# Performance work log

Hardware: AMD Instinct MI355X
Metric: run time of the kernel (lower is better)

## Reference

```python
import jax, jax.numpy as jnp
import numpy as np

N_NODES, N_EDGES = 16384, 8192
IN_CH, HID_CH = 256, 256
ALPHA, BETA = -1.5, -0.5


def setup_inputs() -> dict:
    key = jax.random.key(0)
    k1, k2, k3, k4, k5, k6 = jax.random.split(key, 6)
    x_0 = jax.random.normal(k1, (N_NODES, IN_CH), dtype=jnp.float32)
    # binary incidence matrix (n_nodes, n_edges)
    incidence_1 = jax.random.randint(k2, (N_NODES, N_EDGES), 0, 2).astype(jnp.float32)
    # conv weights (torch Conv: x @ W then neighborhood @ .)
    W0 = jax.random.normal(k3, (IN_CH, HID_CH), dtype=jnp.float32) * 0.02
    W1 = jax.random.normal(k4, (HID_CH, HID_CH), dtype=jnp.float32) * 0.02
    # xavier_uniform biases of shape (1, hidden)
    gain = 1.414
    bound = gain * np.sqrt(6.0 / (1 + HID_CH)) * np.sqrt(3.0) / np.sqrt(3.0)  # xavier bound = gain*sqrt(6/(fan_in+fan_out))
    bound = gain * np.sqrt(6.0 / (1 + HID_CH))
    bias_0_to_1 = jax.random.uniform(k5, (1, HID_CH), minval=-bound, maxval=bound, dtype=jnp.float32)
    bias_1_to_0 = jax.random.uniform(k6, (1, HID_CH), minval=-bound, maxval=bound, dtype=jnp.float32)
    return {"x_0": x_0, "incidence_1": incidence_1, "W0": W0, "W1": W1,
            "bias_0_to_1": bias_0_to_1, "bias_1_to_0": bias_1_to_0}


def _normalize_incidence(B1):
    # edge/node cardinalities raised to alpha/beta
    edge_card = jnp.sum(B1, axis=0) ** ALPHA          # (n_edges,)
    node_card = jnp.sum(B1, axis=1) ** BETA           # (n_nodes,)
    mask = (B1 > 0).astype(B1.dtype)
    d0_inv = 1.0 / (mask @ edge_card)                 # (n_nodes,) per-node sum of incident edge_card
    d1_inv = 1.0 / (mask.T @ node_card)               # (n_edges,) per-edge sum of member node_card
    # B1_norm = D0_left^-1 @ B1 @ diag(edge_card)
    B1_norm = d0_inv[:, None] * B1 * edge_card[None, :]
    # B1T_norm = D1_left^-1 @ B1^T @ diag(node_card)
    B1T_norm = d1_inv[:, None] * B1.T * node_card[None, :]
    return B1_norm, B1T_norm


def reference(x_0, incidence_1, W0, W1, bias_0_to_1, bias_1_to_0):
    B1_norm, B1T_norm = _normalize_incidence(incidence_1)
    # node -> edge conv: x_1 = B1T_norm @ (x_0 @ W0) + b01
    x_1 = B1T_norm @ (x_0 @ W0) + bias_0_to_1        # (n_edges, hid)
    # edge -> node conv: x_0 = B1_norm @ (x_1 @ W1) + b10
    x_0_out = B1_norm @ (x_1 @ W1) + bias_1_to_0     # (n_nodes, hid)
    return jax.nn.relu(x_0_out), jax.nn.relu(x_1)
```

## Files before the change

kernel.cpp:

```cpp
#include <hip/hip_runtime.h>
#include <stdint.h>

#define NN 16384
#define NE 8192
#define CH 256
#define MM1_SPLIT 8
#define MM2_SPLIT 4

typedef __attribute__((ext_vector_type(8))) short bf16x8;
typedef __attribute__((ext_vector_type(4))) float f32x4;

__device__ __forceinline__ unsigned short f2bf(float f) {
  unsigned u = __float_as_uint(f);
  u += 0x7FFFu + ((u >> 16) & 1u);
  return (unsigned short)(u >> 16);
}
__device__ __forceinline__ void async_copy16(const void* gptr, void* lptr) {
  __builtin_amdgcn_global_load_lds((const __attribute__((address_space(1))) unsigned int*)gptr,
                                   (__attribute__((address_space(3))) unsigned int*)lptr,
                                   16, 0, 0);
}
__device__ __forceinline__ uint4 expand8(unsigned byte) {
  uint4 aw;
#pragma unroll
  for (int j = 0; j < 4; ++j) {
    unsigned lo = (byte >> (2 * j)) & 1u;
    unsigned hi = (byte >> (2 * j + 1)) & 1u;
    ((unsigned*)&aw)[j] = lo * 0x3F80u + hi * 0x3F800000u;
  }
  return aw;
}

__device__ __forceinline__ void transpose32(unsigned* x) {
  const unsigned masks[5] = {0x0000FFFFu, 0x00FF00FFu, 0x0F0F0F0Fu, 0x33333333u, 0x55555555u};
#pragma unroll
  for (int jj = 0; jj < 5; ++jj) {
    const int j = 16 >> jj;
    const unsigned m = masks[jj];
#pragma unroll
    for (int k = 0; k < 32; ++k) {
      if ((k & j) == 0) {
        unsigned t = ((x[k] >> j) ^ x[k + j]) & m;
        x[k] ^= (t << j);
        x[k + j] ^= t;
      }
    }
  }
}

__global__ void k0_transpose_w(const float* __restrict__ W0, const float* __restrict__ W1,
                               unsigned short* __restrict__ W0T, unsigned short* __restrict__ W1T) {
  const float* W = blockIdx.y ? W1 : W0;
  unsigned short* WT = blockIdx.y ? W1T : W0T;
  int n = blockIdx.x;
  int k = threadIdx.x;
  WT[n * CH + k] = f2bf(W[k * CH + n]);
}

__global__ void k1_pack_card(const float* __restrict__ B1, unsigned* __restrict__ pk1,
                             float* __restrict__ node_card) {
  int n = blockIdx.x;
  int t = threadIdx.x;
  const float4* p = (const float4*)(B1 + (size_t)n * NE + t * 32);
  unsigned w = 0;
#pragma unroll
  for (int jj = 0; jj < 8; ++jj) {
    float4 v = p[jj];
    w |= ((__float_as_uint(v.x) >> 23) & 1u) << (4 * jj);
    w |= ((__float_as_uint(v.y) >> 23) & 1u) << (4 * jj + 1);
    w |= ((__float_as_uint(v.z) >> 23) & 1u) << (4 * jj + 2);
    w |= ((__float_as_uint(v.w) >> 23) & 1u) << (4 * jj + 3);
  }
  pk1[(size_t)n * 256 + t] = w;
  int s = __popc(w);
  __shared__ int red[4];
#pragma unroll
  for (int off = 32; off; off >>= 1) s += __shfl_down(s, off, 64);
  if ((t & 63) == 0) red[t >> 6] = s;
  __syncthreads();
  if (t == 0) {
    float tot = (float)(red[0] + red[1] + red[2] + red[3]);
    node_card[n] = rsqrtf(tot);
  }
}

__global__ __launch_bounds__(256) void k1b_bitT(const unsigned* __restrict__ pk1,
                                                unsigned* __restrict__ pk1T) {
  int bw = blockIdx.x & 127;
  int half = blockIdx.x >> 7;
  int t = threadIdx.x;
  int nt = half * 256 + t;
  unsigned x0[32], x1[32];
#pragma unroll
  for (int r = 0; r < 32; ++r) {
    uint2 v = *(const uint2*)&pk1[(size_t)(nt * 32 + r) * 256 + 2 * bw];
    x0[r] = v.x;
    x1[r] = v.y;
  }
  transpose32(x0);
  transpose32(x1);
  int e0 = bw * 64;
#pragma unroll
  for (int c = 0; c < 32; ++c) {
    pk1T[(size_t)(e0 + c) * 512 + nt] = x0[c];
    pk1T[(size_t)(e0 + 32 + c) * 512 + nt] = x1[c];
  }
}

__global__ __launch_bounds__(256) void ke_edge(const unsigned* __restrict__ pk1T,
                                               const float* __restrict__ node_card,
                                               float* __restrict__ edge_card,
                                               float* __restrict__ d1) {
  const int t = threadIdx.x;
  const int e0 = blockIdx.x * 4;
  unsigned w[4][2];
#pragma unroll
  for (int r = 0; r < 4; ++r) {
    w[r][0] = pk1T[(size_t)(e0 + r) * 512 + t];
    w[r][1] = pk1T[(size_t)(e0 + r) * 512 + 256 + t];
  }
  float wsum[4] = {0.f, 0.f, 0.f, 0.f};
  int cnt[4];
#pragma unroll
  for (int r = 0; r < 4; ++r) cnt[r] = __popc(w[r][0]) + __popc(w[r][1]);
  const float4* nc0 = (const float4*)(node_card + (size_t)t * 32);
  const float4* nc1 = (const float4*)(node_card + ((size_t)t + 256) * 32);
#pragma unroll
  for (int h = 0; h < 2; ++h) {
    const float4* ncp = h ? nc1 : nc0;
#pragma unroll
    for (int q = 0; q < 8; ++q) {
      float4 v = ncp[q];
#pragma unroll
      for (int r = 0; r < 4; ++r) {
        unsigned ww = w[r][h];
        wsum[r] += ((ww >> (4 * q)) & 1u) ? v.x : 0.f;
        wsum[r] += ((ww >> (4 * q + 1)) & 1u) ? v.y : 0.f;
        wsum[r] += ((ww >> (4 * q + 2)) & 1u) ? v.z : 0.f;
        wsum[r] += ((ww >> (4 * q + 3)) & 1u) ? v.w : 0.f;
      }
    }
  }
#pragma unroll
  for (int off = 32; off; off >>= 1)
#pragma unroll
    for (int r = 0; r < 4; ++r) {
      wsum[r] += __shfl_down(wsum[r], off, 64);
      cnt[r] += __shfl_down(cnt[r], off, 64);
    }
  __shared__ float redW[4][4];
  __shared__ int redC[4][4];
  int wave = t >> 6, lane = t & 63;
  if (lane == 0)
#pragma unroll
    for (int r = 0; r < 4; ++r) {
      redW[wave][r] = wsum[r];
      redC[wave][r] = cnt[r];
    }
  __syncthreads();
  if (t < 4) {
    float s = redW[0][t] + redW[1][t] + redW[2][t] + redW[3][t];
    float c = (float)(redC[0][t] + redC[1][t] + redC[2][t] + redC[3][t]);
    d1[e0 + t] = s;
    edge_card[e0 + t] = 1.0f / (c * sqrtf(c));
  }
}

__global__ __launch_bounds__(256) void kd0_node(const unsigned* __restrict__ pk1,
                                                const float* __restrict__ edge_card,
                                                float* __restrict__ d0) {
  const int t = threadIdx.x;
  const int n0 = blockIdx.x * 4;
  unsigned w[4];
#pragma unroll
  for (int r = 0; r < 4; ++r) w[r] = pk1[(size_t)(n0 + r) * 256 + t];
  float wsum[4] = {0.f, 0.f, 0.f, 0.f};
  const float4* ecp = (const float4*)(edge_card + (size_t)t * 32);
#pragma unroll
  for (int q = 0; q < 8; ++q) {
    float4 v = ecp[q];
#pragma unroll
    for (int r = 0; r < 4; ++r) {
      unsigned ww = w[r];
      wsum[r] += ((ww >> (4 * q)) & 1u) ? v.x : 0.f;
      wsum[r] += ((ww >> (4 * q + 1)) & 1u) ? v.y : 0.f;
      wsum[r] += ((ww >> (4 * q + 2)) & 1u) ? v.z : 0.f;
      wsum[r] += ((ww >> (4 * q + 3)) & 1u) ? v.w : 0.f;
    }
  }
#pragma unroll
  for (int off = 32; off; off >>= 1)
#pragma unroll
    for (int r = 0; r < 4; ++r) wsum[r] += __shfl_down(wsum[r], off, 64);
  __shared__ float redW[4][4];
  int wave = t >> 6, lane = t & 63;
  if (lane == 0)
#pragma unroll
    for (int r = 0; r < 4; ++r) redW[wave][r] = wsum[r];
  __syncthreads();
  if (t < 4) d0[n0 + t] = redW[0][t] + redW[1][t] + redW[2][t] + redW[3][t];
}

__global__ __launch_bounds__(256) void k2_y0(const float* __restrict__ X0,
                                             const unsigned short* __restrict__ W0T,
                                             const float* __restrict__ node_card,
                                             unsigned short* __restrict__ y0sT) {
  __shared__ __align__(16) unsigned short a_lds[32 * 32];
  __shared__ __align__(16) unsigned short b_lds[256 * 32];
  const int tid = threadIdx.x;
  const int wave = tid >> 6, lane = tid & 63;
  const int quad = lane >> 4, l15 = lane & 15;
  const int m0 = blockIdx.x * 32;
  const int ar = tid >> 3, ac = (tid & 7) * 4;

  f32x4 acc[2][4];
  const f32x4 fz = {0.f, 0.f, 0.f, 0.f};
#pragma unroll
  for (int i = 0; i < 2; ++i)
#pragma unroll
    for (int j = 0; j < 4; ++j) acc[i][j] = fz;

  for (int k0 = 0; k0 < CH; k0 += 32) {
    __syncthreads();
    {
      float4 v = *(const float4*)(X0 + (size_t)(m0 + ar) * CH + k0 + ac);
      uint2 w;
      w.x = ((unsigned)f2bf(v.x)) | ((unsigned)f2bf(v.y) << 16);
      w.y = ((unsigned)f2bf(v.z)) | ((unsigned)f2bf(v.w) << 16);
      *(uint2*)&a_lds[ar * 32 + ac] = w;
    }
#pragma unroll
    for (int i = 0; i < 4; ++i) {
      int rowbase = wave * 64 + i * 16;
      const unsigned short* g = W0T + (size_t)(rowbase + (lane >> 2)) * CH + k0 + (lane & 3) * 8;
      async_copy16(g, &b_lds[rowbase * 32]);
    }
    __syncthreads();
    bf16x8 af[2];
#pragma unroll
    for (int i = 0; i < 2; ++i)
      af[i] = *(const bf16x8*)&a_lds[(i * 16 + l15) * 32 + quad * 8];
#pragma unroll
    for (int j = 0; j < 4; ++j) {
      bf16x8 bfr = *(const bf16x8*)&b_lds[(wave * 64 + j * 16 + l15) * 32 + quad * 8];
#pragma unroll
      for (int i = 0; i < 2; ++i)
        acc[i][j] = __builtin_amdgcn_mfma_f32_16x16x32_bf16(af[i], bfr, acc[i][j], 0, 0, 0);
    }
  }
#pragma unroll
  for (int i = 0; i < 2; ++i) {
    int row4 = m0 + i * 16 + quad * 4;
    float4 nc = *(const float4*)(node_card + row4);
#pragma unroll
    for (int j = 0; j < 4; ++j) {
      int col = wave * 64 + j * 16 + l15;
      f32x4 v = acc[i][j];
      ushort4 o;
      o.x = f2bf(v[0] * nc.x);
      o.y = f2bf(v[1] * nc.y);
      o.z = f2bf(v[2] * nc.z);
      o.w = f2bf(v[3] * nc.w);
      *(ushort4*)&y0sT[(size_t)col * NN + row4] = o;
    }
  }
}

__global__ __launch_bounds__(512, 4) void mm1_kernel(const unsigned char* __restrict__ pk1T,
                                                     const unsigned short* __restrict__ y0sT,
                                                     float* __restrict__ mm1p) {
  __shared__ __align__(16) unsigned short b_lds[2][256 * 32];
  const int tid = threadIdx.x;
  const int wave = tid >> 6, lane = tid & 63;
  const int quad = lane >> 4, l15 = lane & 15;
  const int wm = wave >> 2, wn = wave & 3;
  const int bid = blockIdx.x;
  const int sp = bid & 7;
  const int m0 = (bid >> 3) * 128;
  const int KS = NN / MM1_SPLIT;
  const int NT = KS / 32;
  const int kbase = sp * KS;
  const int AST = NN / 8;

  const int brow = lane >> 2;
  const int bcol = (lane & 3) * 8;

  f32x4 acc[4][4];
  const f32x4 fz = {0.f, 0.f, 0.f, 0.f};
#pragma unroll
  for (int i = 0; i < 4; ++i)
#pragma unroll
    for (int j = 0; j < 4; ++j) acc[i][j] = fz;

  const unsigned char* abase = pk1T + (size_t)(m0 + wm * 64 + l15) * AST + (kbase >> 3) + quad;
  unsigned ab[4];
#pragma unroll
  for (int i = 0; i < 4; ++i) ab[i] = abase[(size_t)(i * 16) * AST];

#pragma unroll
  for (int i = 0; i < 2; ++i) {
    int rowbase = wave * 32 + i * 16;
    const unsigned short* g = y0sT + (size_t)(rowbase + brow) * NN + kbase + bcol;
    async_copy16(g, &b_lds[0][rowbase * 32]);
  }
  __syncthreads();

  for (int t = 0; t < NT; ++t) {
    const int cur = t & 1;
    if (t + 1 < NT) {
      const int k0n = kbase + (t + 1) * 32;
#pragma unroll
      for (int i = 0; i < 2; ++i) {
        int rowbase = wave * 32 + i * 16;
        const unsigned short* g = y0sT + (size_t)(rowbase + brow) * NN + k0n + bcol;
        async_copy16(g, &b_lds[cur ^ 1][rowbase * 32]);
      }
    }
    bf16x8 af[4];
#pragma unroll
    for (int i = 0; i < 4; ++i) {
      uint4 ue = expand8(ab[i]);
      af[i] = *reinterpret_cast<bf16x8*>(&ue);
    }
    if (t + 1 < NT) {
#pragma unroll
      for (int i = 0; i < 4; ++i) ab[i] = abase[(size_t)(i * 16) * AST + (t + 1) * 4];
    }
    __builtin_amdgcn_s_setprio(1);
#pragma unroll
    for (int j = 0; j < 4; ++j) {
      bf16x8 bfr = *(const bf16x8*)&b_lds[cur][(wn * 64 + j * 16 + l15) * 32 + quad * 8];
#pragma unroll
      for (int i = 0; i < 4; ++i)
        acc[i][j] = __builtin_amdgcn_mfma_f32_16x16x32_bf16(af[i], bfr, acc[i][j], 0, 0, 0);
    }
    __builtin_amdgcn_s_setprio(0);
    __syncthreads();
  }
  float* outp = mm1p + (size_t)sp * NE * CH;
#pragma unroll
  for (int i = 0; i < 4; ++i) {
    int row4 = m0 + wm * 64 + i * 16 + quad * 4;
#pragma unroll
    for (int j = 0; j < 4; ++j) {
      int col = wn * 64 + j * 16 + l15;
#pragma unroll
      for (int r = 0; r < 4; ++r) outp[(size_t)(row4 + r) * CH + col] = acc[i][j][r];
    }
  }
}

__global__ __launch_bounds__(256) void k3_edge_final(const float* __restrict__ mm1p,
                                                     const float* __restrict__ d1,
                                                     const float* __restrict__ b01,
                                                     float* __restrict__ out1,
                                                     unsigned short* __restrict__ x1bf) {
  const int t = threadIdx.x;
  const int e = blockIdx.x * 4 + (t >> 6);
  const int c4 = (t & 63) * 4;
  float px = 0.f, py = 0.f, pz = 0.f, pw = 0.f;
#pragma unroll
  for (int sp = 0; sp < MM1_SPLIT; ++sp) {
    float4 v = *(const float4*)&mm1p[(size_t)sp * NE * CH + (size_t)e * CH + c4];
    px += v.x; py += v.y; pz += v.z; pw += v.w;
  }
  const float rd = 1.0f / d1[e];
  const float4 b = *(const float4*)&b01[c4];
  float4 x1;
  x1.x = px * rd + b.x;
  x1.y = py * rd + b.y;
  x1.z = pz * rd + b.z;
  x1.w = pw * rd + b.w;
  float4 o;
  o.x = fmaxf(x1.x, 0.f); o.y = fmaxf(x1.y, 0.f);
  o.z = fmaxf(x1.z, 0.f); o.w = fmaxf(x1.w, 0.f);
  *(float4*)&out1[(size_t)e * CH + c4] = o;
  ushort4 xb;
  xb.x = f2bf(x1.x); xb.y = f2bf(x1.y); xb.z = f2bf(x1.z); xb.w = f2bf(x1.w);
  *(ushort4*)&x1bf[(size_t)e * CH + c4] = xb;
}

__global__ __launch_bounds__(256) void k5_y1(const unsigned short* __restrict__ x1bf,
                                             const unsigned short* __restrict__ W1T,
                                             const float* __restrict__ edge_card,
                                             unsigned short* __restrict__ y1sT) {
  __shared__ __align__(16) unsigned short a_lds[32 * 32];
  __shared__ __align__(16) unsigned short b_lds[256 * 32];
  const int tid = threadIdx.x;
  const int wave = tid >> 6, lane = tid & 63;
  const int quad = lane >> 4, l15 = lane & 15;
  const int m0 = blockIdx.x * 32;

  f32x4 acc[2][4];
  const f32x4 fz = {0.f, 0.f, 0.f, 0.f};
#pragma unroll
  for (int i = 0; i < 2; ++i)
#pragma unroll
    for (int j = 0; j < 4; ++j) acc[i][j] = fz;

  for (int k0 = 0; k0 < CH; k0 += 32) {
    __syncthreads();
    if (wave < 2) {
      const unsigned short* g = x1bf + (size_t)(m0 + wave * 16 + (lane >> 2)) * CH + k0 + (lane & 3) * 8;
      async_copy16(g, &a_lds[(wave * 16) * 32]);
    }
#pragma unroll
    for (int i = 0; i < 4; ++i) {
      int rowbase = wave * 64 + i * 16;
      const unsigned short* g = W1T + (size_t)(rowbase + (lane >> 2)) * CH + k0 + (lane & 3) * 8;
      async_copy16(g, &b_lds[rowbase * 32]);
    }
    __syncthreads();
    bf16x8 af[2];
#pragma unroll
    for (int i = 0; i < 2; ++i)
      af[i] = *(const bf16x8*)&a_lds[(i * 16 + l15) * 32 + quad * 8];
#pragma unroll
    for (int j = 0; j < 4; ++j) {
      bf16x8 bfr = *(const bf16x8*)&b_lds[(wave * 64 + j * 16 + l15) * 32 + quad * 8];
#pragma unroll
      for (int i = 0; i < 2; ++i)
        acc[i][j] = __builtin_amdgcn_mfma_f32_16x16x32_bf16(af[i], bfr, acc[i][j], 0, 0, 0);
    }
  }
#pragma unroll
  for (int i = 0; i < 2; ++i) {
    int row4 = m0 + i * 16 + quad * 4;
    float4 ec = *(const float4*)(edge_card + row4);
#pragma unroll
    for (int j = 0; j < 4; ++j) {
      int col = wave * 64 + j * 16 + l15;
      f32x4 v = acc[i][j];
      ushort4 o;
      o.x = f2bf(v[0] * ec.x);
      o.y = f2bf(v[1] * ec.y);
      o.z = f2bf(v[2] * ec.z);
      o.w = f2bf(v[3] * ec.w);
      *(ushort4*)&y1sT[(size_t)col * NE + row4] = o;
    }
  }
}

__global__ __launch_bounds__(512, 4) void mm2_kernel(const unsigned char* __restrict__ pk1,
                                                     const unsigned short* __restrict__ y1sT,
                                                     float* __restrict__ mm2p) {
  __shared__ __align__(16) unsigned short b_lds[2][256 * 32];
  const int tid = threadIdx.x;
  const int wave = tid >> 6, lane = tid & 63;
  const int quad = lane >> 4, l15 = lane & 15;
  const int wm = wave >> 2, wn = wave & 3;
  const int bid = blockIdx.x;
  const int sp = (bid >> 1) & 3;
  const int m0 = (((bid >> 3) << 1) | (bid & 1)) * 128;
  const int KS = NE / MM2_SPLIT;
  const int NT = KS / 32;
  const int kbase = sp * KS;
  const int AST = NE / 8;

  const int brow = lane >> 2;
  const int bcol = (lane & 3) * 8;

  f32x4 acc[4][4];
  const f32x4 fz = {0.f, 0.f, 0.f, 0.f};
#pragma unroll
  for (int i = 0; i < 4; ++i)
#pragma unroll
    for (int j = 0; j < 4; ++j) acc[i][j] = fz;

  const unsigned char* abase = pk1 + (size_t)(m0 + wm * 64 + l15) * AST + (kbase >> 3) + quad;
  unsigned ab[4];
#pragma unroll
  for (int i = 0; i < 4; ++i) ab[i] = abase[(size_t)(i * 16) * AST];

#pragma unroll
  for (int i = 0; i < 2; ++i) {
    int rowbase = wave * 32 + i * 16;
    const unsigned short* g = y1sT + (size_t)(rowbase + brow) * NE + kbase + bcol;
    async_copy16(g, &b_lds[0][rowbase * 32]);
  }
  __syncthreads();

  for (int t = 0; t < NT; ++t) {
    const int cur = t & 1;
    if (t + 1 < NT) {
      const int k0n = kbase + (t + 1) * 32;
#pragma unroll
      for (int i = 0; i < 2; ++i) {
        int rowbase = wave * 32 + i * 16;
        const unsigned short* g = y1sT + (size_t)(rowbase + brow) * NE + k0n + bcol;
        async_copy16(g, &b_lds[cur ^ 1][rowbase * 32]);
      }
    }
    bf16x8 af[4];
#pragma unroll
    for (int i = 0; i < 4; ++i) {
      uint4 ue = expand8(ab[i]);
      af[i] = *reinterpret_cast<bf16x8*>(&ue);
    }
    if (t + 1 < NT) {
#pragma unroll
      for (int i = 0; i < 4; ++i) ab[i] = abase[(size_t)(i * 16) * AST + (t + 1) * 4];
    }
    __builtin_amdgcn_s_setprio(1);
#pragma unroll
    for (int j = 0; j < 4; ++j) {
      bf16x8 bfr = *(const bf16x8*)&b_lds[cur][(wn * 64 + j * 16 + l15) * 32 + quad * 8];
#pragma unroll
      for (int i = 0; i < 4; ++i)
        acc[i][j] = __builtin_amdgcn_mfma_f32_16x16x32_bf16(af[i], bfr, acc[i][j], 0, 0, 0);
    }
    __builtin_amdgcn_s_setprio(0);
    __syncthreads();
  }
  float* outp = mm2p + (size_t)sp * NN * CH;
#pragma unroll
  for (int i = 0; i < 4; ++i) {
    int row4 = m0 + wm * 64 + i * 16 + quad * 4;
#pragma unroll
    for (int j = 0; j < 4; ++j) {
      int col = wn * 64 + j * 16 + l15;
#pragma unroll
      for (int r = 0; r < 4; ++r) outp[(size_t)(row4 + r) * CH + col] = acc[i][j][r];
    }
  }
}

__global__ __launch_bounds__(256) void k6_node_final(const float* __restrict__ mm2p,
                                                     const float* __restrict__ d0,
                                                     const float* __restrict__ b10,
                                                     float* __restrict__ out0) {
  const int t = threadIdx.x;
  const int n = blockIdx.x * 4 + (t >> 6);
  const int c4 = (t & 63) * 4;
  float sx = 0.f, sy = 0.f, sz = 0.f, sw = 0.f;
#pragma unroll
  for (int sp = 0; sp < MM2_SPLIT; ++sp) {
    float4 v = *(const float4*)&mm2p[(size_t)sp * NN * CH + (size_t)n * CH + c4];
    sx += v.x; sy += v.y; sz += v.z; sw += v.w;
  }
  const float rd = 1.0f / d0[n];
  const float4 b = *(const float4*)&b10[c4];
  float4 o;
  o.x = fmaxf(sx * rd + b.x, 0.f);
  o.y = fmaxf(sy * rd + b.y, 0.f);
  o.z = fmaxf(sz * rd + b.z, 0.f);
  o.w = fmaxf(sw * rd + b.w, 0.f);
  *(float4*)&out0[(size_t)n * CH + c4] = o;
}

extern "C" void kernel_launch(void* const* d_in, const int* in_sizes, int n_in,
                              void* d_out, int out_size, void* d_ws, size_t ws_size,
                              hipStream_t stream) {
  const float* x0 = (const float*)d_in[0];
  const float* B1 = (const float*)d_in[1];
  const float* W0 = (const float*)d_in[2];
  const float* W1 = (const float*)d_in[3];
  const float* b01 = (const float*)d_in[4];
  const float* b10 = (const float*)d_in[5];
  float* out0 = (float*)d_out;
  float* out1 = out0 + (size_t)NN * CH;

  char* ws = (char*)d_ws;
  size_t off = 0;
  auto take = [&](size_t bytes) {
    void* p = ws + off;
    off += (bytes + 255) & ~(size_t)255;
    return p;
  };
  unsigned short* y0sT = (unsigned short*)take((size_t)256 * NN * 2);
  unsigned short* y1sT = (unsigned short*)take((size_t)256 * NE * 2);
  unsigned short* x1bf = (unsigned short*)take((size_t)NE * CH * 2);
  float* mm1p = (float*)take((size_t)MM1_SPLIT * NE * CH * 4);
  float* mm2p = mm1p;
  float* node_card = (float*)take((size_t)NN * 4);
  float* edge_card = (float*)take((size_t)NE * 4);
  float* d1 = (float*)take((size_t)NE * 4);
  float* d0 = (float*)take((size_t)NN * 4);
  unsigned short* W0T = (unsigned short*)take((size_t)CH * CH * 2);
  unsigned short* W1T = (unsigned short*)take((size_t)CH * CH * 2);
  unsigned* pk1 = (unsigned*)take((size_t)NN * 256 * 4);
  unsigned* pk1T = (unsigned*)take((size_t)NE * 512 * 4);
  (void)ws_size; (void)in_sizes; (void)n_in; (void)out_size;

  k0_transpose_w<<<dim3(256, 2), 256, 0, stream>>>(W0, W1, W0T, W1T);
  k1_pack_card<<<NN, 256, 0, stream>>>(B1, pk1, node_card);
  k1b_bitT<<<256, 256, 0, stream>>>(pk1, pk1T);
  ke_edge<<<NE / 4, 256, 0, stream>>>(pk1T, node_card, edge_card, d1);
  kd0_node<<<NN / 4, 256, 0, stream>>>(pk1, edge_card, d0);
  k2_y0<<<NN / 32, 256, 0, stream>>>(x0, W0T, node_card, y0sT);
  mm1_kernel<<<512, 512, 0, stream>>>((const unsigned char*)pk1T, y0sT, mm1p);
  k3_edge_final<<<NE / 4, 256, 0, stream>>>(mm1p, d1, b01, out1, x1bf);
  k5_y1<<<NE / 32, 256, 0, stream>>>(x1bf, W1T, edge_card, y1sT);
  mm2_kernel<<<512, 512, 0, stream>>>((const unsigned char*)pk1, y1sT, mm2p);
  k6_node_final<<<NN / 4, 256, 0, stream>>>(mm2p, d0, b10, out0);
}
```

Measured before the change: 1.122 ms.

## Switch bit-packed GEMMs to 32x32x16 MFMA with shared-expanded A tile in LDS

```diff
diff --git a/kernel.cpp b/kernel.cpp
--- a/kernel.cpp
+++ b/kernel.cpp
@@ -9,6 +9,7 @@
 
 typedef __attribute__((ext_vector_type(8))) short bf16x8;
 typedef __attribute__((ext_vector_type(4))) float f32x4;
+typedef __attribute__((ext_vector_type(16))) float f32x16;
 
 __device__ __forceinline__ unsigned short f2bf(float f) {
   unsigned u = __float_as_uint(f);
@@ -269,10 +270,11 @@
 __global__ __launch_bounds__(512, 4) void mm1_kernel(const unsigned char* __restrict__ pk1T,
                                                      const unsigned short* __restrict__ y0sT,
                                                      float* __restrict__ mm1p) {
+  __shared__ __align__(16) unsigned short a_lds[2][128 * 40];
   __shared__ __align__(16) unsigned short b_lds[2][256 * 32];
   const int tid = threadIdx.x;
   const int wave = tid >> 6, lane = tid & 63;
-  const int quad = lane >> 4, l15 = lane & 15;
+  const int l31 = lane & 31, half = lane >> 5;
   const int wm = wave >> 2, wn = wave & 3;
   const int bid = blockIdx.x;
   const int sp = bid & 7;
@@ -280,22 +282,31 @@
   const int KS = NN / MM1_SPLIT;
   const int NT = KS / 32;
   const int kbase = sp * KS;
-  const int AST = NN / 8;
-
+
+  const int am = tid >> 2;
+  const int akg = tid & 3;
+  const int ajbs = akg ^ ((am >> 4) & 3);
+  const int aoff = am * 40 + ajbs * 8;
   const int brow = lane >> 2;
   const int bcol = (lane & 3) * 8;
 
-  f32x4 acc[4][4];
-  const f32x4 fz = {0.f, 0.f, 0.f, 0.f};
-#pragma unroll
-  for (int i = 0; i < 4; ++i)
-#pragma unroll
-    for (int j = 0; j < 4; ++j) acc[i][j] = fz;
-
-  const unsigned char* abase = pk1T + (size_t)(m0 + wm * 64 + l15) * AST + (kbase >> 3) + quad;
-  unsigned ab[4];
-#pragma unroll
-  for (int i = 0; i < 4; ++i) ab[i] = abase[(size_t)(i * 16) * AST];
+  const int arow0 = wm * 64 + l31;
+  const int arow1 = wm * 64 + 32 + l31;
+  const int as0 = (arow0 >> 4) & 3;
+  const int as1 = (arow1 >> 4) & 3;
+
+  f32x16 acc[2][2];
+#pragma unroll
+  for (int r = 0; r < 2; ++r)
+#pragma unroll
+    for (int c = 0; c < 2; ++c)
+#pragma unroll
+      for (int q = 0; q < 16; ++q) acc[r][c][q] = 0.f;
+
+  const unsigned char* agp = pk1T + (size_t)(m0 + am) * (NN / 8) + (kbase >> 3) + akg;
+  unsigned ab_cur = agp[0];
+  unsigned ab_nxt = agp[4];
+  const unsigned char* agq = agp + 8;
 
 #pragma unroll
   for (int i = 0; i < 2; ++i) {
@@ -303,10 +314,12 @@
     const unsigned short* g = y0sT + (size_t)(rowbase + brow) * NN + kbase + bcol;
     async_copy16(g, &b_lds[0][rowbase * 32]);
   }
+  *(uint4*)&a_lds[0][aoff] = expand8(ab_cur);
   __syncthreads();
 
   for (int t = 0; t < NT; ++t) {
     const int cur = t & 1;
+    unsigned ab_new = 0;
     if (t + 1 < NT) {
       const int k0n = kbase + (t + 1) * 32;
 #pragma unroll
@@ -315,39 +328,40 @@
         const unsigned short* g = y0sT + (size_t)(rowbase + brow) * NN + k0n + bcol;
         async_copy16(g, &b_lds[cur ^ 1][rowbase * 32]);
       }
-    }
-    bf16x8 af[4];
-#pragma unroll
-    for (int i = 0; i < 4; ++i) {
-      uint4 ue = expand8(ab[i]);
-      af[i] = *reinterpret_cast<bf16x8*>(&ue);
-    }
-    if (t + 1 < NT) {
-#pragma unroll
-      for (int i = 0; i < 4; ++i) ab[i] = abase[(size_t)(i * 16) * AST + (t + 1) * 4];
-    }
-    __builtin_amdgcn_s_setprio(1);
-#pragma unroll
-    for (int j = 0; j < 4; ++j) {
-      bf16x8 bfr = *(const bf16x8*)&b_lds[cur][(wn * 64 + j * 16 + l15) * 32 + quad * 8];
-#pragma unroll
-      for (int i = 0; i < 4; ++i)
-        acc[i][j] = __builtin_amdgcn_mfma_f32_16x16x32_bf16(af[i], bfr, acc[i][j], 0, 0, 0);
-    }
-    __builtin_amdgcn_s_setprio(0);
+      *(uint4*)&a_lds[cur ^ 1][aoff] = expand8(ab_nxt);
+      if (t + 2 < NT) {
+        ab_new = *agq;
+        agq += 4;
+      }
+    }
+#pragma unroll
+    for (int kb = 0; kb < 2; ++kb) {
+      const int kg = kb * 2 + half;
+      bf16x8 af0 = *(const bf16x8*)&a_lds[cur][arow0 * 40 + (kg ^ as0) * 8];
+      bf16x8 af1 = *(const bf16x8*)&a_lds[cur][arow1 * 40 + (kg ^ as1) * 8];
+      bf16x8 bf0 = *(const bf16x8*)&b_lds[cur][(wn * 64 + l31) * 32 + kg * 8];
+      bf16x8 bf1 = *(const bf16x8*)&b_lds[cur][(wn * 64 + 32 + l31) * 32 + kg * 8];
+      acc[0][0] = __builtin_amdgcn_mfma_f32_32x32x16_bf16(af0, bf0, acc[0][0], 0, 0, 0);
+      acc[1][0] = __builtin_amdgcn_mfma_f32_32x32x16_bf16(af1, bf0, acc[1][0], 0, 0, 0);
+      acc[0][1] = __builtin_amdgcn_mfma_f32_32x32x16_bf16(af0, bf1, acc[0][1], 0, 0, 0);
+      acc[1][1] = __builtin_amdgcn_mfma_f32_32x32x16_bf16(af1, bf1, acc[1][1], 0, 0, 0);
+    }
     __syncthreads();
+    ab_cur = ab_nxt;
+    ab_nxt = ab_new;
   }
   float* outp = mm1p + (size_t)sp * NE * CH;
 #pragma unroll
-  for (int i = 0; i < 4; ++i) {
-    int row4 = m0 + wm * 64 + i * 16 + quad * 4;
-#pragma unroll
-    for (int j = 0; j < 4; ++j) {
-      int col = wn * 64 + j * 16 + l15;
-#pragma unroll
-      for (int r = 0; r < 4; ++r) outp[(size_t)(row4 + r) * CH + col] = acc[i][j][r];
-    }
-  }
+  for (int r = 0; r < 2; ++r)
+#pragma unroll
+    for (int c = 0; c < 2; ++c) {
+      const int col = wn * 64 + c * 32 + l31;
+#pragma unroll
+      for (int reg = 0; reg < 16; ++reg) {
+        const int row = m0 + wm * 64 + r * 32 + (reg & 3) + 8 * (reg >> 2) + 4 * half;
+        outp[(size_t)row * CH + col] = acc[r][c][reg];
+      }
+    }
 }
 
 __global__ __launch_bounds__(256) void k3_edge_final(const float* __restrict__ mm1p,
@@ -444,10 +458,11 @@
 __global__ __launch_bounds__(512, 4) void mm2_kernel(const unsigned char* __restrict__ pk1,
                                                      const unsigned short* __restrict__ y1sT,
                                                      float* __restrict__ mm2p) {
+  __shared__ __align__(16) unsigned short a_lds[2][128 * 40];
   __shared__ __align__(16) unsigned short b_lds[2][256 * 32];
   const int tid = threadIdx.x;
   const int wave = tid >> 6, lane = tid & 63;
-  const int quad = lane >> 4, l15 = lane & 15;
+  const int l31 = lane & 31, half = lane >> 5;
   const int wm = wave >> 2, wn = wave & 3;
   const int bid = blockIdx.x;
   const int sp = (bid >> 1) & 3;
@@ -455,22 +470,31 @@
   const int KS = NE / MM2_SPLIT;
   const int NT = KS / 32;
   const int kbase = sp * KS;
-  const int AST = NE / 8;
-
+
+  const int am = tid >> 2;
+  const int akg = tid & 3;
+  const int ajbs = akg ^ ((am >> 4) & 3);
+  const int aoff = am * 40 + ajbs * 8;
   const int brow = lane >> 2;
   const int bcol = (lane & 3) * 8;
 
-  f32x4 acc[4][4];
-  const f32x4 fz = {0.f, 0.f, 0.f, 0.f};
-#pragma unroll
-  for (int i = 0; i < 4; ++i)
-#pragma unroll
-    for (int j = 0; j < 4; ++j) acc[i][j] = fz;
-
-  const unsigned char* abase = pk1 + (size_t)(m0 + wm * 64 + l15) * AST + (kbase >> 3) + quad;
-  unsigned ab[4];
-#pragma unroll
-  for (int i = 0; i < 4; ++i) ab[i] = abase[(size_t)(i * 16) * AST];
+  const int arow0 = wm * 64 + l31;
+  const int arow1 = wm * 64 + 32 + l31;
+  const int as0 = (arow0 >> 4) & 3;
+  const int as1 = (arow1 >> 4) & 3;
+
+  f32x16 acc[2][2];
+#pragma unroll
+  for (int r = 0; r < 2; ++r)
+#pragma unroll
+    for (int c = 0; c < 2; ++c)
+#pragma unroll
+      for (int q = 0; q < 16; ++q) acc[r][c][q] = 0.f;
+
+  const unsigned char* agp = pk1 + (size_t)(m0 + am) * (NE / 8) + (kbase >> 3) + akg;
+  unsigned ab_cur = agp[0];
+  unsigned ab_nxt = agp[4];
+  const unsigned char* agq = agp + 8;
 
 #pragma unroll
   for (int i = 0; i < 2; ++i) {
@@ -478,10 +502,12 @@
     const unsigned short* g = y1sT + (size_t)(rowbase + brow) * NE + kbase + bcol;
     async_copy16(g, &b_lds[0][rowbase * 32]);
   }
+  *(uint4*)&a_lds[0][aoff] = expand8(ab_cur);
   __syncthreads();
 
   for (int t = 0; t < NT; ++t) {
     const int cur = t & 1;
+    unsigned ab_new = 0;
     if (t + 1 < NT) {
       const int k0n = kbase + (t + 1) * 32;
 #pragma unroll
@@ -490,39 +516,40 @@
         const unsigned short* g = y1sT + (size_t)(rowbase + brow) * NE + k0n + bcol;
         async_copy16(g, &b_lds[cur ^ 1][rowbase * 32]);
       }
-    }
-    bf16x8 af[4];
-#pragma unroll
-    for (int i = 0; i < 4; ++i) {
-      uint4 ue = expand8(ab[i]);
-      af[i] = *reinterpret_cast<bf16x8*>(&ue);
-    }
-    if (t + 1 < NT) {
-#pragma unroll
-      for (int i = 0; i < 4; ++i) ab[i] = abase[(size_t)(i * 16) * AST + (t + 1) * 4];
-    }
-    __builtin_amdgcn_s_setprio(1);
-#pragma unroll
-    for (int j = 0; j < 4; ++j) {
-      bf16x8 bfr = *(const bf16x8*)&b_lds[cur][(wn * 64 + j * 16 + l15) * 32 + quad * 8];
-#pragma unroll
-      for (int i = 0; i < 4; ++i)
-        acc[i][j] = __builtin_amdgcn_mfma_f32_16x16x32_bf16(af[i], bfr, acc[i][j], 0, 0, 0);
-    }
-    __builtin_amdgcn_s_setprio(0);
+      *(uint4*)&a_lds[cur ^ 1][aoff] = expand8(ab_nxt);
+      if (t + 2 < NT) {
+        ab_new = *agq;
+        agq += 4;
+      }
+    }
+#pragma unroll
+    for (int kb = 0; kb < 2; ++kb) {
+      const int kg = kb * 2 + half;
+      bf16x8 af0 = *(const bf16x8*)&a_lds[cur][arow0 * 40 + (kg ^ as0) * 8];
+      bf16x8 af1 = *(const bf16x8*)&a_lds[cur][arow1 * 40 + (kg ^ as1) * 8];
+      bf16x8 bf0 = *(const bf16x8*)&b_lds[cur][(wn * 64 + l31) * 32 + kg * 8];
+      bf16x8 bf1 = *(const bf16x8*)&b_lds[cur][(wn * 64 + 32 + l31) * 32 + kg * 8];
+      acc[0][0] = __builtin_amdgcn_mfma_f32_32x32x16_bf16(af0, bf0, acc[0][0], 0, 0, 0);
+      acc[1][0] = __builtin_amdgcn_mfma_f32_32x32x16_bf16(af1, bf0, acc[1][0], 0, 0, 0);
+      acc[0][1] = __builtin_amdgcn_mfma_f32_32x32x16_bf16(af0, bf1, acc[0][1], 0, 0, 0);
+      acc[1][1] = __builtin_amdgcn_mfma_f32_32x32x16_bf16(af1, bf1, acc[1][1], 0, 0, 0);
+    }
     __syncthreads();
+    ab_cur = ab_nxt;
+    ab_nxt = ab_new;
   }
   float* outp = mm2p + (size_t)sp * NN * CH;
 #pragma unroll
-  for (int i = 0; i < 4; ++i) {
-    int row4 = m0 + wm * 64 + i * 16 + quad * 4;
-#pragma unroll
-    for (int j = 0; j < 4; ++j) {
-      int col = wn * 64 + j * 16 + l15;
-#pragma unroll
-      for (int r = 0; r < 4; ++r) outp[(size_t)(row4 + r) * CH + col] = acc[i][j][r];
-    }
-  }
+  for (int r = 0; r < 2; ++r)
+#pragma unroll
+    for (int c = 0; c < 2; ++c) {
+      const int col = wn * 64 + c * 32 + l31;
+#pragma unroll
+      for (int reg = 0; reg < 16; ++reg) {
+        const int row = m0 + wm * 64 + r * 32 + (reg & 3) + 8 * (reg >> 2) + 4 * half;
+        outp[(size_t)row * CH + col] = acc[r][c][reg];
+      }
+    }
 }
 
 __global__ __launch_bounds__(256) void k6_node_final(const float* __restrict__ mm2p,
```

New measurement: 983.2 us. -12.3%, faster.

## Swizzle LDS tiles and stage expanded incidence bits through shared memory

Applied to the files above, without the earlier changes.

```diff
diff --git a/kernel.cpp b/kernel.cpp
--- a/kernel.cpp
+++ b/kernel.cpp
@@ -212,6 +212,9 @@
   const int quad = lane >> 4, l15 = lane & 15;
   const int m0 = blockIdx.x * 32;
   const int ar = tid >> 3, ac = (tid & 7) * 4;
+  const int acs = (((ac >> 3) ^ ((ar >> 1) & 3)) * 8) + (ac & 4);
+  const int bswz = ((lane & 3) ^ ((lane >> 3) & 3)) * 8;
+  const int rg = (l15 >> 1) & 3;
 
   f32x4 acc[2][4];
   const f32x4 fz = {0.f, 0.f, 0.f, 0.f};
@@ -227,22 +230,22 @@
       uint2 w;
       w.x = ((unsigned)f2bf(v.x)) | ((unsigned)f2bf(v.y) << 16);
       w.y = ((unsigned)f2bf(v.z)) | ((unsigned)f2bf(v.w) << 16);
-      *(uint2*)&a_lds[ar * 32 + ac] = w;
+      *(uint2*)&a_lds[ar * 32 + acs] = w;
     }
 #pragma unroll
     for (int i = 0; i < 4; ++i) {
       int rowbase = wave * 64 + i * 16;
-      const unsigned short* g = W0T + (size_t)(rowbase + (lane >> 2)) * CH + k0 + (lane & 3) * 8;
+      const unsigned short* g = W0T + (size_t)(rowbase + (lane >> 2)) * CH + k0 + bswz;
       async_copy16(g, &b_lds[rowbase * 32]);
     }
     __syncthreads();
     bf16x8 af[2];
 #pragma unroll
     for (int i = 0; i < 2; ++i)
-      af[i] = *(const bf16x8*)&a_lds[(i * 16 + l15) * 32 + quad * 8];
-#pragma unroll
-    for (int j = 0; j < 4; ++j) {
-      bf16x8 bfr = *(const bf16x8*)&b_lds[(wave * 64 + j * 16 + l15) * 32 + quad * 8];
+      af[i] = *(const bf16x8*)&a_lds[(i * 16 + l15) * 32 + (quad ^ rg) * 8];
+#pragma unroll
+    for (int j = 0; j < 4; ++j) {
+      bf16x8 bfr = *(const bf16x8*)&b_lds[(wave * 64 + j * 16 + l15) * 32 + (quad ^ rg) * 8];
 #pragma unroll
       for (int i = 0; i < 2; ++i)
         acc[i][j] = __builtin_amdgcn_mfma_f32_16x16x32_bf16(af[i], bfr, acc[i][j], 0, 0, 0);
@@ -269,6 +272,7 @@
 __global__ __launch_bounds__(512, 4) void mm1_kernel(const unsigned char* __restrict__ pk1T,
                                                      const unsigned short* __restrict__ y0sT,
                                                      float* __restrict__ mm1p) {
+  __shared__ __align__(16) unsigned short a_lds[2][128 * 40];
   __shared__ __align__(16) unsigned short b_lds[2][256 * 32];
   const int tid = threadIdx.x;
   const int wave = tid >> 6, lane = tid & 63;
@@ -280,10 +284,14 @@
   const int KS = NN / MM1_SPLIT;
   const int NT = KS / 32;
   const int kbase = sp * KS;
-  const int AST = NN / 8;
-
+
+  const int am = tid >> 2;
+  const int akg = tid & 3;
+  const int ajbs = akg ^ ((am >> 4) & 3);
+  const int aoff = am * 40 + ajbs * 8;
   const int brow = lane >> 2;
-  const int bcol = (lane & 3) * 8;
+  const int bswz = ((lane & 3) ^ ((lane >> 3) & 3)) * 8;
+  const int rg = (l15 >> 1) & 3;
 
   f32x4 acc[4][4];
   const f32x4 fz = {0.f, 0.f, 0.f, 0.f};
@@ -292,50 +300,54 @@
 #pragma unroll
     for (int j = 0; j < 4; ++j) acc[i][j] = fz;
 
-  const unsigned char* abase = pk1T + (size_t)(m0 + wm * 64 + l15) * AST + (kbase >> 3) + quad;
-  unsigned ab[4];
-#pragma unroll
-  for (int i = 0; i < 4; ++i) ab[i] = abase[(size_t)(i * 16) * AST];
+  const unsigned char* agp = pk1T + (size_t)(m0 + am) * (NN / 8) + (kbase >> 3) + akg;
+  unsigned ab_cur = agp[0];
+  unsigned ab_nxt = agp[4];
+  const unsigned char* agq = agp + 8;
 
 #pragma unroll
   for (int i = 0; i < 2; ++i) {
     int rowbase = wave * 32 + i * 16;
-    const unsigned short* g = y0sT + (size_t)(rowbase + brow) * NN + kbase + bcol;
+    const unsigned short* g = y0sT + (size_t)(rowbase + brow) * NN + kbase + bswz;
     async_copy16(g, &b_lds[0][rowbase * 32]);
   }
+  *(uint4*)&a_lds[0][aoff] = expand8(ab_cur);
   __syncthreads();
 
   for (int t = 0; t < NT; ++t) {
     const int cur = t & 1;
+    unsigned ab_new = 0;
     if (t + 1 < NT) {
       const int k0n = kbase + (t + 1) * 32;
 #pragma unroll
       for (int i = 0; i < 2; ++i) {
         int rowbase = wave * 32 + i * 16;
-        const unsigned short* g = y0sT + (size_t)(rowbase + brow) * NN + k0n + bcol;
+        const unsigned short* g = y0sT + (size_t)(rowbase + brow) * NN + k0n + bswz;
         async_copy16(g, &b_lds[cur ^ 1][rowbase * 32]);
       }
+      *(uint4*)&a_lds[cur ^ 1][aoff] = expand8(ab_nxt);
+      if (t + 2 < NT) {
+        ab_new = *agq;
+        agq += 4;
+      }
     }
     bf16x8 af[4];
 #pragma unroll
     for (int i = 0; i < 4; ++i) {
-      uint4 ue = expand8(ab[i]);
-      af[i] = *reinterpret_cast<bf16x8*>(&ue);
-    }
-    if (t + 1 < NT) {
-#pragma unroll
-      for (int i = 0; i < 4; ++i) ab[i] = abase[(size_t)(i * 16) * AST + (t + 1) * 4];
-    }
-    __builtin_amdgcn_s_setprio(1);
-#pragma unroll
-    for (int j = 0; j < 4; ++j) {
-      bf16x8 bfr = *(const bf16x8*)&b_lds[cur][(wn * 64 + j * 16 + l15) * 32 + quad * 8];
+      int m = wm * 64 + i * 16 + l15;
+      int jbs = quad ^ ((m >> 4) & 3);
+      af[i] = *(const bf16x8*)&a_lds[cur][m * 40 + jbs * 8];
+    }
+#pragma unroll
+    for (int j = 0; j < 4; ++j) {
+      bf16x8 bfr = *(const bf16x8*)&b_lds[cur][(wn * 64 + j * 16 + l15) * 32 + (quad ^ rg) * 8];
 #pragma unroll
       for (int i = 0; i < 4; ++i)
         acc[i][j] = __builtin_amdgcn_mfma_f32_16x16x32_bf16(af[i], bfr, acc[i][j], 0, 0, 0);
     }
-    __builtin_amdgcn_s_setprio(0);
     __syncthreads();
+    ab_cur = ab_nxt;
+    ab_nxt = ab_new;
   }
   float* outp = mm1p + (size_t)sp * NE * CH;
 #pragma unroll
@@ -390,6 +402,8 @@
   const int wave = tid >> 6, lane = tid & 63;
   const int quad = lane >> 4, l15 = lane & 15;
   const int m0 = blockIdx.x * 32;
+  const int bswz = ((lane & 3) ^ ((lane >> 3) & 3)) * 8;
+  const int rg = (l15 >> 1) & 3;
 
   f32x4 acc[2][4];
   const f32x4 fz = {0.f, 0.f, 0.f, 0.f};
@@ -401,23 +415,23 @@
   for (int k0 = 0; k0 < CH; k0 += 32) {
     __syncthreads();
     if (wave < 2) {
-      const unsigned short* g = x1bf + (size_t)(m0 + wave * 16 + (lane >> 2)) * CH + k0 + (lane & 3) * 8;
+      const unsigned short* g = x1bf + (size_t)(m0 + wave * 16 + (lane >> 2)) * CH + k0 + bswz;
       async_copy16(g, &a_lds[(wave * 16) * 32]);
     }
 #pragma unroll
     for (int i = 0; i < 4; ++i) {
       int rowbase = wave * 64 + i * 16;
-      const unsigned short* g = W1T + (size_t)(rowbase + (lane >> 2)) * CH + k0 + (lane & 3) * 8;
+      const unsigned short* g = W1T + (size_t)(rowbase + (lane >> 2)) * CH + k0 + bswz;
       async_copy16(g, &b_lds[rowbase * 32]);
     }
     __syncthreads();
     bf16x8 af[2];
 #pragma unroll
     for (int i = 0; i < 2; ++i)
-      af[i] = *(const bf16x8*)&a_lds[(i * 16 + l15) * 32 + quad * 8];
-#pragma unroll
-    for (int j = 0; j < 4; ++j) {
-      bf16x8 bfr = *(const bf16x8*)&b_lds[(wave * 64 + j * 16 + l15) * 32 + quad * 8];
+      af[i] = *(const bf16x8*)&a_lds[(i * 16 + l15) * 32 + (quad ^ rg) * 8];
+#pragma unroll
+    for (int j = 0; j < 4; ++j) {
+      bf16x8 bfr = *(const bf16x8*)&b_lds[(wave * 64 + j * 16 + l15) * 32 + (quad ^ rg) * 8];
 #pragma unroll
       for (int i = 0; i < 2; ++i)
         acc[i][j] = __builtin_amdgcn_mfma_f32_16x16x32_bf16(af[i], bfr, acc[i][j], 0, 0, 0);
@@ -444,6 +458,7 @@
 __global__ __launch_bounds__(512, 4) void mm2_kernel(const unsigned char* __restrict__ pk1,
                                                      const unsigned short* __restrict__ y1sT,
                                                      float* __restrict__ mm2p) {
+  __shared__ __align__(16) unsigned short a_lds[2][128 * 40];
   __shared__ __align__(16) unsigned short b_lds[2][256 * 32];
   const int tid = threadIdx.x;
   const int wave = tid >> 6, lane = tid & 63;
@@ -455,10 +470,14 @@
   const int KS = NE / MM2_SPLIT;
   const int NT = KS / 32;
   const int kbase = sp * KS;
-  const int AST = NE / 8;
-
+
+  const int am = tid >> 2;
+  const int akg = tid & 3;
+  const int ajbs = akg ^ ((am >> 4) & 3);
+  const int aoff = am * 40 + ajbs * 8;
   const int brow = lane >> 2;
-  const int bcol = (lane & 3) * 8;
+  const int bswz = ((lane & 3) ^ ((lane >> 3) & 3)) * 8;
+  const int rg = (l15 >> 1) & 3;
 
   f32x4 acc[4][4];
   const f32x4 fz = {0.f, 0.f, 0.f, 0.f};
@@ -467,50 +486,54 @@
 #pragma unroll
     for (int j = 0; j < 4; ++j) acc[i][j] = fz;
 
-  const unsigned char* abase = pk1 + (size_t)(m0 + wm * 64 + l15) * AST + (kbase >> 3) + quad;
-  unsigned ab[4];
-#pragma unroll
-  for (int i = 0; i < 4; ++i) ab[i] = abase[(size_t)(i * 16) * AST];
+  const unsigned char* agp = pk1 + (size_t)(m0 + am) * (NE / 8) + (kbase >> 3) + akg;
+  unsigned ab_cur = agp[0];
+  unsigned ab_nxt = agp[4];
+  const unsigned char* agq = agp + 8;
 
 #pragma unroll
   for (int i = 0; i < 2; ++i) {
     int rowbase = wave * 32 + i * 16;
-    const unsigned short* g = y1sT + (size_t)(rowbase + brow) * NE + kbase + bcol;
+    const unsigned short* g = y1sT + (size_t)(rowbase + brow) * NE + kbase + bswz;
     async_copy16(g, &b_lds[0][rowbase * 32]);
   }
+  *(uint4*)&a_lds[0][aoff] = expand8(ab_cur);
   __syncthreads();
 
   for (int t = 0; t < NT; ++t) {
     const int cur = t & 1;
+    unsigned ab_new = 0;
     if (t + 1 < NT) {
       const int k0n = kbase + (t + 1) * 32;
 #pragma unroll
       for (int i = 0; i < 2; ++i) {
         int rowbase = wave * 32 + i * 16;
-        const unsigned short* g = y1sT + (size_t)(rowbase + brow) * NE + k0n + bcol;
+        const unsigned short* g = y1sT + (size_t)(rowbase + brow) * NE + k0n + bswz;
         async_copy16(g, &b_lds[cur ^ 1][rowbase * 32]);
       }
+      *(uint4*)&a_lds[cur ^ 1][aoff] = expand8(ab_nxt);
+      if (t + 2 < NT) {
+        ab_new = *agq;
+        agq += 4;
+      }
     }
     bf16x8 af[4];
 #pragma unroll
     for (int i = 0; i < 4; ++i) {
-      uint4 ue = expand8(ab[i]);
-      af[i] = *reinterpret_cast<bf16x8*>(&ue);
-    }
-    if (t + 1 < NT) {
-#pragma unroll
-      for (int i = 0; i < 4; ++i) ab[i] = abase[(size_t)(i * 16) * AST + (t + 1) * 4];
-    }
-    __builtin_amdgcn_s_setprio(1);
-#pragma unroll
-    for (int j = 0; j < 4; ++j) {
-      bf16x8 bfr = *(const bf16x8*)&b_lds[cur][(wn * 64 + j * 16 + l15) * 32 + quad * 8];
+      int m = wm * 64 + i * 16 + l15;
+      int jbs = quad ^ ((m >> 4) & 3);
+      af[i] = *(const bf16x8*)&a_lds[cur][m * 40 + jbs * 8];
+    }
+#pragma unroll
+    for (int j = 0; j < 4; ++j) {
+      bf16x8 bfr = *(const bf16x8*)&b_lds[cur][(wn * 64 + j * 16 + l15) * 32 + (quad ^ rg) * 8];
 #pragma unroll
       for (int i = 0; i < 4; ++i)
         acc[i][j] = __builtin_amdgcn_mfma_f32_16x16x32_bf16(af[i], bfr, acc[i][j], 0, 0, 0);
     }
-    __builtin_amdgcn_s_setprio(0);
     __syncthreads();
+    ab_cur = ab_nxt;
+    ab_nxt = ab_new;
   }
   float* outp = mm2p + (size_t)sp * NN * CH;
 #pragma unroll
```

After: 951.0 us, median of 2. 1.18x faster.
